# Kernel optimization log

Hardware: AMD Instinct MI355X
Metric: run time of the kernel (lower is better)

Reference implementation:

```python
import jax, jax.numpy as jnp
import numpy as np

BLOCK = 64          # block_dim
GAPS = (1, 64)      # block_dim**i for i in range(num_layers=2), input_dim=4096
N_BLOCKS = 64       # input_dim // block_dim
HID = 128           # 2 * block_dim (hidden_layers_ratio=[2])
BS = 8192
IN_DIM = 4096


def setup_inputs() -> dict:
    key = jax.random.key(0)
    kx, kw1, kw2 = jax.random.split(key, 3)
    x = jax.random.normal(kx, (BS, IN_DIM), dtype=jnp.float32)
    # one BlockResMLP per factorized layer: BlockLinear(64, 64, 128) -> ELU -> BlockLinear(64, 128, 64)
    w1 = jax.random.normal(kw1, (len(GAPS), N_BLOCKS, BLOCK, HID), dtype=jnp.float32) / np.sqrt(BLOCK)
    b1 = jnp.zeros((len(GAPS), N_BLOCKS, 1, HID), dtype=jnp.float32)
    w2 = jax.random.normal(kw2, (len(GAPS), N_BLOCKS, HID, BLOCK), dtype=jnp.float32) / np.sqrt(HID)
    b2 = jnp.zeros((len(GAPS), N_BLOCKS, 1, BLOCK), dtype=jnp.float32)
    return {"x": x, "w1": w1, "b1": b1, "w2": w2, "b2": b2}


def _facto(y, w1, b1, w2, b2):
    # BlockResMLP.forward: view(bs, n_blocks, BLOCK).transpose(0,1) -> batched block GEMMs -> residual
    bs = y.shape[0]
    z = y.reshape(bs, -1, BLOCK).transpose(1, 0, 2)              # (n_blocks, bs, BLOCK)
    h = jnp.einsum('nbd,nde->nbe', z, w1) + b1                   # BlockLinear 1 + bias
    h = jax.nn.elu(h)                                            # ELU (alpha=1)
    h = jnp.einsum('nbe,ned->nbd', h, w2) + b2                   # BlockLinear 2 + bias
    z = h + z                                                    # residual
    return z.transpose(1, 0, 2).reshape(bs, -1)


def reference(x, w1, b1, w2, b2):
    bs = x.shape[0]
    y = x
    for i, gap in enumerate(GAPS):
        # permutation shuffle: view(-1, BLOCK, gap).transpose(2,1).contiguous().view(bs,-1)
        y = y.reshape(-1, BLOCK, gap).transpose(0, 2, 1).reshape(bs, -1)
        y = _facto(y, w1[i], b1[i], w2[i], b2[i])
        # inverse shuffle: view(-1, gap, BLOCK).transpose(2,1)
        y = y.reshape(-1, gap, BLOCK).transpose(0, 2, 1).reshape(bs, -1)
    return y
```

## Files before the change

kernel.cpp:

```cpp
#include <hip/hip_runtime.h>


typedef short short8 __attribute__((ext_vector_type(8)));
typedef float floatx4 __attribute__((ext_vector_type(4)));

#define MFMA(A, B, C) __builtin_amdgcn_mfma_f32_16x16x32_bf16((A), (B), (C), 0, 0, 0)

__device__ __forceinline__ unsigned short bf16r(float f) {
  unsigned int u = __builtin_bit_cast(unsigned int, f);
  u += 0x7FFFu + ((u >> 16) & 1u);
  return (unsigned short)(u >> 16);
}
__device__ __forceinline__ float bf16f(unsigned short h) {
  unsigned int u = ((unsigned int)h) << 16;
  return __builtin_bit_cast(float, u);
}
__device__ __forceinline__ float eluf(float v) {
  return v > 0.f ? v : (__expf(v) - 1.f);
}

__global__ __launch_bounds__(256) void k0_prep(const float* __restrict__ w1,
                                               const float* __restrict__ w2,
                                               short* __restrict__ w1t,
                                               short* __restrict__ w2t) {
  int tid = blockIdx.x * 256 + threadIdx.x;
  int d  = tid & 63;
  int e  = (tid >> 6) & 127;
  int ln = tid >> 13;
  w1t[tid] = (short)bf16r(w1[((size_t)ln * 64 + d) * 128 + e]);
  int e2 = tid & 127;
  int dp = (tid >> 7) & 63;
  w2t[tid] = (short)bf16r(w2[((size_t)ln * 128 + e2) * 64 + dp]);
}

__global__ __launch_bounds__(256) void k1_layer0(
    const float* __restrict__ x,
    const short* __restrict__ w1t, const short* __restrict__ w2t,
    const float* __restrict__ b1,  const float* __restrict__ b2,
    short* __restrict__ y1) {
  __shared__ __align__(16) short hst[4][2][16][72];
  const int tid  = threadIdx.x;
  const int lane = tid & 63;
  const int wv   = tid >> 6;
  const int il   = lane & 15;
  const int q    = lane >> 4;
  const int npair   = blockIdx.x & 31;
  const int rowtile = blockIdx.x >> 5;
  const int n  = npair * 2 + (wv & 1);
  const int r0 = rowtile * 64 + (wv >> 1) * 32;

  const short* w1n = w1t + (size_t)n * 8192;
  const short* w2n = w2t + (size_t)n * 8192;
  const float* b1n = b1 + n * 128;
  const float* b2n = b2 + n * 64;

  short8 a[2][2];
#pragma unroll
  for (int Mt = 0; Mt < 2; ++Mt) {
#pragma unroll
    for (int ks = 0; ks < 2; ++ks) {
      const float* xp = x + (size_t)(r0 + Mt * 16 + il) * 4096 + n * 64 + ks * 32 + q * 8;
      floatx4 f0 = *(const floatx4*)xp;
      floatx4 f1 = *(const floatx4*)(xp + 4);
      short8 t;
#pragma unroll
      for (int u = 0; u < 4; ++u) { t[u] = (short)bf16r(f0[u]); t[4 + u] = (short)bf16r(f1[u]); }
      a[ks][Mt] = t;
    }
  }

  floatx4 acc2[2][4] = {};
  for (int hh = 0; hh < 2; ++hh) {
    floatx4 acc1[2][4] = {};
#pragma unroll
    for (int ks = 0; ks < 2; ++ks) {
#pragma unroll
      for (int nt = 0; nt < 4; ++nt) {
        short8 b = *(const short8*)(w1n + (hh * 64 + nt * 16 + il) * 64 + ks * 32 + q * 8);
        acc1[0][nt] = MFMA(a[ks][0], b, acc1[0][nt]);
        acc1[1][nt] = MFMA(a[ks][1], b, acc1[1][nt]);
      }
    }
#pragma unroll
    for (int nt = 0; nt < 4; ++nt) {
      float bias = b1n[hh * 64 + nt * 16 + il];
#pragma unroll
      for (int Mt = 0; Mt < 2; ++Mt)
#pragma unroll
        for (int rg = 0; rg < 4; ++rg) {
          float v = acc1[Mt][nt][rg] + bias;
          hst[wv][Mt][q * 4 + rg][nt * 16 + il] = (short)bf16r(eluf(v));
        }
    }
    asm volatile("s_waitcnt lgkmcnt(0)" ::: "memory");
#pragma unroll
    for (int ks2 = 0; ks2 < 2; ++ks2) {
      short8 a2[2];
      a2[0] = *(const short8*)&hst[wv][0][il][ks2 * 32 + q * 8];
      a2[1] = *(const short8*)&hst[wv][1][il][ks2 * 32 + q * 8];
#pragma unroll
      for (int nt2 = 0; nt2 < 4; ++nt2) {
        short8 b = *(const short8*)(w2n + (nt2 * 16 + il) * 128 + hh * 64 + ks2 * 32 + q * 8);
        acc2[0][nt2] = MFMA(a2[0], b, acc2[0][nt2]);
        acc2[1][nt2] = MFMA(a2[1], b, acc2[1][nt2]);
      }
    }
    asm volatile("s_waitcnt lgkmcnt(0)" ::: "memory");
  }
  const size_t nbase = ((size_t)(r0 >> 5) * 64 + n) * 64;
#pragma unroll
  for (int Mt = 0; Mt < 2; ++Mt) {
    const int R0 = r0 + Mt * 16 + q * 4;
#pragma unroll
    for (int nt2 = 0; nt2 < 4; ++nt2) {
      const int j = nt2 * 16 + il;
      const float bias = b2n[j];
      float v0 = acc2[Mt][nt2][0] + bias + x[(size_t)(R0 + 0) * 4096 + n * 64 + j];
      float v1 = acc2[Mt][nt2][1] + bias + x[(size_t)(R0 + 1) * 4096 + n * 64 + j];
      float v2 = acc2[Mt][nt2][2] + bias + x[(size_t)(R0 + 2) * 4096 + n * 64 + j];
      float v3 = acc2[Mt][nt2][3] + bias + x[(size_t)(R0 + 3) * 4096 + n * 64 + j];
      uint2 pk;
      pk.x = (unsigned int)bf16r(v0) | ((unsigned int)bf16r(v1) << 16);
      pk.y = (unsigned int)bf16r(v2) | ((unsigned int)bf16r(v3) << 16);
      *(uint2*)(y1 + (nbase + j) * 32 + Mt * 16 + q * 4) = pk;
    }
  }
}

__global__ __launch_bounds__(256) void k2_layer1(
    const short* __restrict__ y1,
    const short* __restrict__ w1t, const short* __restrict__ w2t,
    const float* __restrict__ b1,  const float* __restrict__ b2,
    short* __restrict__ y2) {
  __shared__ __align__(16) short zL[64][72];
  __shared__ __align__(16) short hs[4][16][72];
  const int tid  = threadIdx.x;
  const int lane = tid & 63;
  const int wv   = tid >> 6;
  const int il   = lane & 15;
  const int q    = lane >> 4;
  const int m  = blockIdx.x & 63;
  const int R0 = (blockIdx.x >> 6) * 64;

  {
    const int i    = tid & 63;
    const int half = tid >> 6;
    const short* src = y1 + (((size_t)((R0 >> 5) + (half >> 1)) * 64 + i) * 64 + m) * 32 + (half & 1) * 16;
    uint4 v0 = *(const uint4*)src;
    uint4 v1 = *(const uint4*)(src + 8);
    const short* p0 = (const short*)&v0;
    const short* p1 = (const short*)&v1;
#pragma unroll
    for (int k = 0; k < 8; ++k) zL[half * 16 + k][i] = p0[k];
#pragma unroll
    for (int k = 0; k < 8; ++k) zL[half * 16 + 8 + k][i] = p1[k];
  }
  __syncthreads();

  const int mrow = wv * 16;
  const short* w1m = w1t + (size_t)(64 + m) * 8192;
  const short* w2m = w2t + (size_t)(64 + m) * 8192;
  const float* b1m = b1 + (64 + m) * 128;
  const float* b2m = b2 + (64 + m) * 64;

  floatx4 acc2[4] = {};
  for (int hh = 0; hh < 2; ++hh) {
    floatx4 acc1[4] = {};
#pragma unroll
    for (int ks = 0; ks < 2; ++ks) {
      short8 a = *(const short8*)&zL[mrow + il][ks * 32 + q * 8];
#pragma unroll
      for (int nt = 0; nt < 4; ++nt) {
        short8 b = *(const short8*)(w1m + (hh * 64 + nt * 16 + il) * 64 + ks * 32 + q * 8);
        acc1[nt] = MFMA(a, b, acc1[nt]);
      }
    }
#pragma unroll
    for (int nt = 0; nt < 4; ++nt) {
      float bias = b1m[hh * 64 + nt * 16 + il];
#pragma unroll
      for (int rg = 0; rg < 4; ++rg) {
        hs[wv][q * 4 + rg][nt * 16 + il] = (short)bf16r(eluf(acc1[nt][rg] + bias));
      }
    }
    asm volatile("s_waitcnt lgkmcnt(0)" ::: "memory");
#pragma unroll
    for (int ks2 = 0; ks2 < 2; ++ks2) {
      short8 a2 = *(const short8*)&hs[wv][il][ks2 * 32 + q * 8];
#pragma unroll
      for (int nt2 = 0; nt2 < 4; ++nt2) {
        short8 b = *(const short8*)(w2m + (nt2 * 16 + il) * 128 + hh * 64 + ks2 * 32 + q * 8);
        acc2[nt2] = MFMA(a2, b, acc2[nt2]);
      }
    }
    asm volatile("s_waitcnt lgkmcnt(0)" ::: "memory");
  }
#pragma unroll
  for (int nt2 = 0; nt2 < 4; ++nt2) {
    const int j = nt2 * 16 + il;
    const float bias = b2m[j];
#pragma unroll
    for (int k = 0; k < 4; ++k) {
      float r = bf16f((unsigned short)zL[mrow + q * 4 + k][j]);
      hs[wv][q * 4 + k][j] = (short)bf16r(acc2[nt2][k] + bias + r);
    }
  }
  asm volatile("s_waitcnt lgkmcnt(0)" ::: "memory");
  const int rr = lane & 15;
  const int iq = lane >> 4;
#pragma unroll
  for (int t = 0; t < 4; ++t) {
    const uint2 v = *(const uint2*)&hs[wv][rr][t * 16 + iq * 4];
    *(uint2*)(y2 + ((size_t)(m * 8192 + R0 + mrow + rr)) * 64 + t * 16 + iq * 4) = v;
  }
}

__global__ __launch_bounds__(256) void k3_unshuffle(
    const short* __restrict__ y2, float* __restrict__ out) {
  __shared__ __align__(16) short st[4][64][68];
  const int tid  = threadIdx.x;
  const int lane = tid & 63;
  const int wv   = tid >> 6;
  const int R    = blockIdx.x * 4 + wv;
  const int mq = lane >> 2;
  const int iq = lane & 3;
#pragma unroll
  for (int mt = 0; mt < 4; ++mt) {
#pragma unroll
    for (int it = 0; it < 4; ++it) {
      const int mm = mt * 16 + mq;
      const int i  = it * 16 + iq * 4;
      const uint2 v = *(const uint2*)(y2 + ((size_t)(mm * 8192 + R)) * 64 + i);
      *(uint2*)&st[wv][mm][i] = v;
    }
  }
  asm volatile("s_waitcnt vmcnt(0) lgkmcnt(0)" ::: "memory");
  float* orow = out + (size_t)R * 4096;
#pragma unroll 4
  for (int i = 0; i < 64; ++i) {
    orow[i * 64 + lane] = bf16f((unsigned short)st[wv][lane][i]);
  }
}

extern "C" void kernel_launch(void* const* d_in, const int* in_sizes, int n_in,
                              void* d_out, int out_size, void* d_ws, size_t ws_size,
                              hipStream_t stream) {
  const float* x  = (const float*)d_in[0];
  const float* w1 = (const float*)d_in[1];
  const float* b1 = (const float*)d_in[2];
  const float* w2 = (const float*)d_in[3];
  const float* b2 = (const float*)d_in[4];
  float* out = (float*)d_out;

  short* w1t = (short*)d_ws;
  short* w2t = w1t + (1u << 20);
  short* y1  = w2t + (1u << 20);
  short* y2  = y1 + (1ull << 25);

  hipLaunchKernelGGL(k0_prep,      dim3(4096), dim3(256), 0, stream, w1, w2, w1t, w2t);
  hipLaunchKernelGGL(k1_layer0,    dim3(4096), dim3(256), 0, stream, x, w1t, w2t, b1, b2, y1);
  hipLaunchKernelGGL(k2_layer1,    dim3(8192), dim3(256), 0, stream, y1, w1t, w2t, b1, b2, y2);
  hipLaunchKernelGGL(k3_unshuffle, dim3(2048), dim3(256), 0, stream, y2, out);
}
```

Before: 466.5 us.

## Fuse layer-1 MLP with unshuffle output and tile weight-prep transpose via LDS

The layer-1 block MLP and the final unshuffle are merged into one kernel. Each block processes 16 rows across 16 block-indices, keeps the results in LDS and writes fp32 output directly, so the intermediate bf16 y2 buffer is never written to or re-read from global memory. The y1 layout changes to 16-row tiles to suit the new gather pattern. Weight prep now uses an LDS-staged transpose with coalesced reads and vector writes. In exchange, each block uses much more LDS (about 37KB), which may lower occupancy.

```diff
diff --git a/kernel.cpp b/kernel.cpp
--- a/kernel.cpp
+++ b/kernel.cpp
@@ -18,19 +18,57 @@
 __device__ __forceinline__ float eluf(float v) {
   return v > 0.f ? v : (__expf(v) - 1.f);
 }
+__device__ __forceinline__ uint4 gather8(const short* base, int stride) {
+  uint4 o;
+  o.x = (unsigned int)(unsigned short)base[0 * stride] |
+        ((unsigned int)(unsigned short)base[1 * stride] << 16);
+  o.y = (unsigned int)(unsigned short)base[2 * stride] |
+        ((unsigned int)(unsigned short)base[3 * stride] << 16);
+  o.z = (unsigned int)(unsigned short)base[4 * stride] |
+        ((unsigned int)(unsigned short)base[5 * stride] << 16);
+  o.w = (unsigned int)(unsigned short)base[6 * stride] |
+        ((unsigned int)(unsigned short)base[7 * stride] << 16);
+  return o;
+}
 
 __global__ __launch_bounds__(256) void k0_prep(const float* __restrict__ w1,
                                                const float* __restrict__ w2,
                                                short* __restrict__ w1t,
                                                short* __restrict__ w2t) {
-  int tid = blockIdx.x * 256 + threadIdx.x;
-  int d  = tid & 63;
-  int e  = (tid >> 6) & 127;
-  int ln = tid >> 13;
-  w1t[tid] = (short)bf16r(w1[((size_t)ln * 64 + d) * 128 + e]);
-  int e2 = tid & 127;
-  int dp = (tid >> 7) & 63;
-  w2t[tid] = (short)bf16r(w2[((size_t)ln * 128 + e2) * 64 + dp]);
+  __shared__ __align__(16) short T[128 * 72];
+  const int t  = threadIdx.x;
+  const int ln = blockIdx.x >> 1;
+  if ((blockIdx.x & 1) == 0) {
+    const float* src = w1 + (size_t)ln * 8192 + t * 32;
+    const int d = t >> 2, e0 = (t & 3) * 32;
+#pragma unroll
+    for (int u = 0; u < 32; u += 2) {
+      float f0 = src[u], f1 = src[u + 1];
+      unsigned int pk = (unsigned int)bf16r(f0) | ((unsigned int)bf16r(f1) << 16);
+      *(unsigned int*)&T[d * 136 + e0 + u] = pk;
+    }
+    __syncthreads();
+    const int e = t >> 1, d0 = (t & 1) * 32;
+    short* dst = w1t + (size_t)ln * 8192 + e * 64 + d0;
+#pragma unroll
+    for (int k = 0; k < 4; ++k)
+      *(uint4*)(dst + k * 8) = gather8(&T[(d0 + k * 8) * 136 + e], 136);
+  } else {
+    const float* src = w2 + (size_t)ln * 8192 + t * 32;
+    const int e = t >> 1, d0 = (t & 1) * 32;
+#pragma unroll
+    for (int u = 0; u < 32; u += 2) {
+      float f0 = src[u], f1 = src[u + 1];
+      unsigned int pk = (unsigned int)bf16r(f0) | ((unsigned int)bf16r(f1) << 16);
+      *(unsigned int*)&T[e * 72 + d0 + u] = pk;
+    }
+    __syncthreads();
+    const int dp = t >> 2, e0 = (t & 3) * 32;
+    short* dst = w2t + (size_t)ln * 8192 + dp * 128 + e0;
+#pragma unroll
+    for (int k = 0; k < 4; ++k)
+      *(uint4*)(dst + k * 8) = gather8(&T[(e0 + k * 8) * 72 + dp], 72);
+  }
 }
 
 __global__ __launch_bounds__(256) void k1_layer0(
@@ -107,10 +145,10 @@
     }
     asm volatile("s_waitcnt lgkmcnt(0)" ::: "memory");
   }
-  const size_t nbase = ((size_t)(r0 >> 5) * 64 + n) * 64;
 #pragma unroll
   for (int Mt = 0; Mt < 2; ++Mt) {
     const int R0 = r0 + Mt * 16 + q * 4;
+    const size_t nbase = ((size_t)((r0 + Mt * 16) >> 4) * 64 + n) * 64;
 #pragma unroll
     for (int nt2 = 0; nt2 < 4; ++nt2) {
       const int j = nt2 * 16 + il;
@@ -122,123 +160,120 @@
       uint2 pk;
       pk.x = (unsigned int)bf16r(v0) | ((unsigned int)bf16r(v1) << 16);
       pk.y = (unsigned int)bf16r(v2) | ((unsigned int)bf16r(v3) << 16);
-      *(uint2*)(y1 + (nbase + j) * 32 + Mt * 16 + q * 4) = pk;
-    }
-  }
-}
-
-__global__ __launch_bounds__(256) void k2_layer1(
+      *(uint2*)(y1 + (nbase + j) * 16 + q * 4) = pk;
+    }
+  }
+}
+
+__global__ __launch_bounds__(256) void k2_layer1_out(
     const short* __restrict__ y1,
     const short* __restrict__ w1t, const short* __restrict__ w2t,
     const float* __restrict__ b1,  const float* __restrict__ b2,
-    short* __restrict__ y2) {
-  __shared__ __align__(16) short zL[64][72];
+    float* __restrict__ out) {
+  __shared__ __align__(16) short zL2[16 * 1160];
   __shared__ __align__(16) short hs[4][16][72];
   const int tid  = threadIdx.x;
   const int lane = tid & 63;
   const int wv   = tid >> 6;
   const int il   = lane & 15;
   const int q    = lane >> 4;
-  const int m  = blockIdx.x & 63;
-  const int R0 = (blockIdx.x >> 6) * 64;
+  const int rt16 = blockIdx.x & 511;
+  const int m0   = (blockIdx.x >> 9) * 16;
 
   {
-    const int i    = tid & 63;
-    const int half = tid >> 6;
-    const short* src = y1 + (((size_t)((R0 >> 5) + (half >> 1)) * 64 + i) * 64 + m) * 32 + (half & 1) * 16;
-    uint4 v0 = *(const uint4*)src;
-    uint4 v1 = *(const uint4*)(src + 8);
-    const short* p0 = (const short*)&v0;
-    const short* p1 = (const short*)&v1;
-#pragma unroll
-    for (int k = 0; k < 8; ++k) zL[half * 16 + k][i] = p0[k];
-#pragma unroll
-    for (int k = 0; k < 8; ++k) zL[half * 16 + 8 + k][i] = p1[k];
+    const int i   = tid >> 2;
+    const int sub = tid & 3;
+    const short* src = y1 + ((size_t)(rt16 * 64 + i) * 64 + m0 + sub * 4) * 16;
+#pragma unroll
+    for (int j = 0; j < 8; ++j) {
+      uint4 w = *(const uint4*)(src + j * 8);
+      const int mm = j >> 1;
+      const int rb = (j & 1) * 8;
+      unsigned int c[4] = {w.x, w.y, w.z, w.w};
+      short* zb = zL2 + (sub * 4 + mm) * 1160 + i;
+#pragma unroll
+      for (int h = 0; h < 4; ++h) {
+        zb[(rb + h * 2 + 0) * 72] = (short)(c[h] & 0xffffu);
+        zb[(rb + h * 2 + 1) * 72] = (short)(c[h] >> 16);
+      }
+    }
   }
   __syncthreads();
 
-  const int mrow = wv * 16;
-  const short* w1m = w1t + (size_t)(64 + m) * 8192;
-  const short* w2m = w2t + (size_t)(64 + m) * 8192;
-  const float* b1m = b1 + (64 + m) * 128;
-  const float* b2m = b2 + (64 + m) * 64;
-
-  floatx4 acc2[4] = {};
-  for (int hh = 0; hh < 2; ++hh) {
-    floatx4 acc1[4] = {};
-#pragma unroll
-    for (int ks = 0; ks < 2; ++ks) {
-      short8 a = *(const short8*)&zL[mrow + il][ks * 32 + q * 8];
+#pragma unroll
+  for (int mi = 0; mi < 4; ++mi) {
+    const int ml = wv * 4 + mi;
+    const int m  = m0 + ml;
+    const short* w1m = w1t + (size_t)(64 + m) * 8192;
+    const short* w2m = w2t + (size_t)(64 + m) * 8192;
+    const float* b1m = b1 + (64 + m) * 128;
+    const float* b2m = b2 + (64 + m) * 64;
+    short* zrow = zL2 + ml * 1160;
+
+    floatx4 acc2[4] = {};
+    for (int hh = 0; hh < 2; ++hh) {
+      floatx4 acc1[4] = {};
+#pragma unroll
+      for (int ks = 0; ks < 2; ++ks) {
+        short8 a = *(const short8*)(zrow + il * 72 + ks * 32 + q * 8);
+#pragma unroll
+        for (int nt = 0; nt < 4; ++nt) {
+          short8 b = *(const short8*)(w1m + (hh * 64 + nt * 16 + il) * 64 + ks * 32 + q * 8);
+          acc1[nt] = MFMA(a, b, acc1[nt]);
+        }
+      }
 #pragma unroll
       for (int nt = 0; nt < 4; ++nt) {
-        short8 b = *(const short8*)(w1m + (hh * 64 + nt * 16 + il) * 64 + ks * 32 + q * 8);
-        acc1[nt] = MFMA(a, b, acc1[nt]);
-      }
-    }
-#pragma unroll
-    for (int nt = 0; nt < 4; ++nt) {
-      float bias = b1m[hh * 64 + nt * 16 + il];
-#pragma unroll
-      for (int rg = 0; rg < 4; ++rg) {
-        hs[wv][q * 4 + rg][nt * 16 + il] = (short)bf16r(eluf(acc1[nt][rg] + bias));
-      }
-    }
-    asm volatile("s_waitcnt lgkmcnt(0)" ::: "memory");
-#pragma unroll
-    for (int ks2 = 0; ks2 < 2; ++ks2) {
-      short8 a2 = *(const short8*)&hs[wv][il][ks2 * 32 + q * 8];
-#pragma unroll
-      for (int nt2 = 0; nt2 < 4; ++nt2) {
-        short8 b = *(const short8*)(w2m + (nt2 * 16 + il) * 128 + hh * 64 + ks2 * 32 + q * 8);
-        acc2[nt2] = MFMA(a2, b, acc2[nt2]);
-      }
-    }
-    asm volatile("s_waitcnt lgkmcnt(0)" ::: "memory");
-  }
-#pragma unroll
-  for (int nt2 = 0; nt2 < 4; ++nt2) {
-    const int j = nt2 * 16 + il;
-    const float bias = b2m[j];
-#pragma unroll
-    for (int k = 0; k < 4; ++k) {
-      float r = bf16f((unsigned short)zL[mrow + q * 4 + k][j]);
-      hs[wv][q * 4 + k][j] = (short)bf16r(acc2[nt2][k] + bias + r);
-    }
-  }
-  asm volatile("s_waitcnt lgkmcnt(0)" ::: "memory");
-  const int rr = lane & 15;
-  const int iq = lane >> 4;
-#pragma unroll
-  for (int t = 0; t < 4; ++t) {
-    const uint2 v = *(const uint2*)&hs[wv][rr][t * 16 + iq * 4];
-    *(uint2*)(y2 + ((size_t)(m * 8192 + R0 + mrow + rr)) * 64 + t * 16 + iq * 4) = v;
-  }
-}
-
-__global__ __launch_bounds__(256) void k3_unshuffle(
-    const short* __restrict__ y2, float* __restrict__ out) {
-  __shared__ __align__(16) short st[4][64][68];
-  const int tid  = threadIdx.x;
-  const int lane = tid & 63;
-  const int wv   = tid >> 6;
-  const int R    = blockIdx.x * 4 + wv;
-  const int mq = lane >> 2;
-  const int iq = lane & 3;
-#pragma unroll
-  for (int mt = 0; mt < 4; ++mt) {
-#pragma unroll
-    for (int it = 0; it < 4; ++it) {
-      const int mm = mt * 16 + mq;
-      const int i  = it * 16 + iq * 4;
-      const uint2 v = *(const uint2*)(y2 + ((size_t)(mm * 8192 + R)) * 64 + i);
-      *(uint2*)&st[wv][mm][i] = v;
-    }
-  }
-  asm volatile("s_waitcnt vmcnt(0) lgkmcnt(0)" ::: "memory");
-  float* orow = out + (size_t)R * 4096;
-#pragma unroll 4
-  for (int i = 0; i < 64; ++i) {
-    orow[i * 64 + lane] = bf16f((unsigned short)st[wv][lane][i]);
+        float bias = b1m[hh * 64 + nt * 16 + il];
+#pragma unroll
+        for (int rg = 0; rg < 4; ++rg)
+          hs[wv][q * 4 + rg][nt * 16 + il] = (short)bf16r(eluf(acc1[nt][rg] + bias));
+      }
+      asm volatile("s_waitcnt lgkmcnt(0)" ::: "memory");
+#pragma unroll
+      for (int ks2 = 0; ks2 < 2; ++ks2) {
+        short8 a2 = *(const short8*)&hs[wv][il][ks2 * 32 + q * 8];
+#pragma unroll
+        for (int nt2 = 0; nt2 < 4; ++nt2) {
+          short8 b = *(const short8*)(w2m + (nt2 * 16 + il) * 128 + hh * 64 + ks2 * 32 + q * 8);
+          acc2[nt2] = MFMA(a2, b, acc2[nt2]);
+        }
+      }
+      asm volatile("s_waitcnt lgkmcnt(0)" ::: "memory");
+    }
+#pragma unroll
+    for (int nt2 = 0; nt2 < 4; ++nt2) {
+      const int i = nt2 * 16 + il;
+      const float bias = b2m[i];
+#pragma unroll
+      for (int k = 0; k < 4; ++k) {
+        short* slot = zrow + (q * 4 + k) * 72 + i;
+        float r = bf16f((unsigned short)*slot);
+        *slot = (short)bf16r(acc2[nt2][k] + bias + r);
+      }
+    }
+  }
+  __syncthreads();
+
+  const int r = tid >> 4;
+  const int c = tid & 15;
+  float* orow = out + (size_t)(rt16 * 16 + r) * 4096 + m0;
+#pragma unroll
+  for (int k = 0; k < 4; ++k) {
+    const int i = c * 4 + k;
+    float vv[16];
+#pragma unroll
+    for (int ml = 0; ml < 16; ++ml)
+      vv[ml] = bf16f((unsigned short)zL2[ml * 1160 + r * 72 + i]);
+    float* op = orow + i * 64;
+    floatx4 a0 = {vv[0],  vv[1],  vv[2],  vv[3]};
+    floatx4 a1 = {vv[4],  vv[5],  vv[6],  vv[7]};
+    floatx4 a2 = {vv[8],  vv[9],  vv[10], vv[11]};
+    floatx4 a3 = {vv[12], vv[13], vv[14], vv[15]};
+    *(floatx4*)(op + 0)  = a0;
+    *(floatx4*)(op + 4)  = a1;
+    *(floatx4*)(op + 8)  = a2;
+    *(floatx4*)(op + 12) = a3;
   }
 }
 
@@ -255,10 +290,8 @@
   short* w1t = (short*)d_ws;
   short* w2t = w1t + (1u << 20);
   short* y1  = w2t + (1u << 20);
-  short* y2  = y1 + (1ull << 25);
-
-  hipLaunchKernelGGL(k0_prep,      dim3(4096), dim3(256), 0, stream, w1, w2, w1t, w2t);
-  hipLaunchKernelGGL(k1_layer0,    dim3(4096), dim3(256), 0, stream, x, w1t, w2t, b1, b2, y1);
-  hipLaunchKernelGGL(k2_layer1,    dim3(8192), dim3(256), 0, stream, y1, w1t, w2t, b1, b2, y2);
-  hipLaunchKernelGGL(k3_unshuffle, dim3(2048), dim3(256), 0, stream, y2, out);
-}
+
+  hipLaunchKernelGGL(k0_prep,       dim3(256),  dim3(256), 0, stream, w1, w2, w1t, w2t);
+  hipLaunchKernelGGL(k1_layer0,     dim3(4096), dim3(256), 0, stream, x, w1t, w2t, b1, b2, y1);
+  hipLaunchKernelGGL(k2_layer1_out, dim3(2048), dim3(256), 0, stream, y1, w1t, w2t, b1, b2, out);
+}
```

New measurement: 453.8 us. 2.7% less time.
